# Kernel optimization log

Hardware: AMD Instinct MI355X
Metric: run time of the kernel (lower is better)

The kernel has to match this reference:

```python
import jax, jax.numpy as jnp
import numpy as np
import math

D_MODEL = 1024
N_HEADS = 16
HEAD_DIM = D_MODEL // N_HEADS
SEQ_LEN = 8192
INCLUDE_LOCAL = 2


def get_dilated_positions(seq_len, include_local=2):
    # Faithful numpy port of the torch pattern generator (runs once at setup).
    max_attend = include_local + int(math.ceil(math.log2(seq_len + 1)))
    positions = np.zeros((seq_len, max_attend), dtype=np.int64)
    mask = np.zeros((seq_len, max_attend), dtype=bool)
    for i in range(seq_len):
        ap = [i]
        for j in range(1, include_local + 1):
            if i - j >= 0:
                ap.append(i - j)
        k = 2
        while i - 2 ** k >= 0:
            ap.append(i - 2 ** k)
            k += 1
        positions[i, :len(ap)] = ap
        mask[i, :len(ap)] = True
    return positions, mask


def setup_inputs() -> dict:
    key = jax.random.key(0)
    kx, kq, kk, kv, ko = jax.random.split(key, 5)
    x = jax.random.normal(kx, (1, SEQ_LEN, D_MODEL), dtype=jnp.float32)
    # nn.Linear(bias=False) weights, torch layout [out_features, in_features]
    s = 0.02
    q_w = jax.random.normal(kq, (D_MODEL, D_MODEL), dtype=jnp.float32) * s
    k_w = jax.random.normal(kk, (D_MODEL, D_MODEL), dtype=jnp.float32) * s
    v_w = jax.random.normal(kv, (D_MODEL, D_MODEL), dtype=jnp.float32) * s
    o_w = jax.random.normal(ko, (D_MODEL, D_MODEL), dtype=jnp.float32) * s
    pos_np, mask_np = get_dilated_positions(SEQ_LEN, INCLUDE_LOCAL)
    return {
        "x": x,
        "q_w": q_w, "k_w": k_w, "v_w": v_w, "o_w": o_w,
        "positions": jnp.asarray(pos_np),   # (S, A) int64 indices
        "attend_mask": jnp.asarray(mask_np) # (S, A) bool
    }


def reference(x, q_w, k_w, v_w, o_w, positions, attend_mask):
    B, S, _ = x.shape
    H, Dh = N_HEADS, HEAD_DIM
    scale = Dh ** -0.5

    q = (x @ q_w.T).reshape(B, S, H, Dh).transpose(0, 2, 1, 3)  # (B,H,S,Dh)
    k = (x @ k_w.T).reshape(B, S, H, Dh).transpose(0, 2, 1, 3)
    v = (x @ v_w.T).reshape(B, S, H, Dh).transpose(0, 2, 1, 3)

    # Gather K/V at the dilated positions: (B,H,S,A,Dh)
    k_sparse = k[:, :, positions, :]
    v_sparse = v[:, :, positions, :]

    scores = jnp.einsum('bhsd,bhsad->bhsa', q, k_sparse) * scale
    scores = jnp.where(attend_mask[None, None, :, :], scores, -jnp.inf)
    attn = jax.nn.softmax(scores, axis=-1)  # dropout p in eval / 0.0 -> identity

    out = jnp.einsum('bhsa,bhsad->bhsd', attn, v_sparse)
    out = out.transpose(0, 2, 1, 3).reshape(B, S, D_MODEL)
    return out @ o_w.T
```

## Files before the change

### kernel.cpp

```cpp
#include <hip/hip_runtime.h>
#include <hip/hip_bf16.h>

typedef __bf16 bf16_t;
typedef __bf16 bf16x4 __attribute__((ext_vector_type(4)));
typedef __bf16 bf16x8 __attribute__((ext_vector_type(8)));
typedef float floatx4 __attribute__((ext_vector_type(4)));

#define SEQ    8192
#define DM     1024
#define NHEADS 16
#define HDIM   64

__device__ __forceinline__ void async_ld16(bf16_t* lds, const bf16_t* g) {
  __builtin_amdgcn_global_load_lds(
      (__attribute__((address_space(1))) void*)g,
      (__attribute__((address_space(3))) void*)lds, 16, 0, 0);
}

__global__ __launch_bounds__(256)
void cvt_all(const float* __restrict__ x,  const float* __restrict__ qw,
             const float* __restrict__ kw, const float* __restrict__ vw,
             const float* __restrict__ ow,
             bf16_t* __restrict__ Xb,  bf16_t* __restrict__ QWb,
             bf16_t* __restrict__ KWb, bf16_t* __restrict__ VWb,
             bf16_t* __restrict__ OWb) {
  const int b = blockIdx.x;
  const float* in; bf16_t* out; int g;
  if (b < 8192) { in = x; out = Xb; g = b; }
  else {
    const int w  = (b - 8192) >> 10;
    const int wb = (b - 8192) & 1023;
    switch (w) {
      case 0:  in = qw; out = QWb; break;
      case 1:  in = kw; out = KWb; break;
      case 2:  in = vw; out = VWb; break;
      default: in = ow; out = OWb; break;
    }
    g = wb;
  }
  const int idx = (g * 256 + threadIdx.x) * 4;
  float4 v = *(const float4*)(in + idx);
  bf16x4 o = { (bf16_t)v.x, (bf16_t)v.y, (bf16_t)v.z, (bf16_t)v.w };
  *(bf16x4*)(out + idx) = o;
}


__global__ __launch_bounds__(256)
void gemm_qkv(const bf16_t* __restrict__ A,
              const bf16_t* __restrict__ Bq, const bf16_t* __restrict__ Bk,
              const bf16_t* __restrict__ Bv,
              bf16_t* __restrict__ Cq, bf16_t* __restrict__ Ck, bf16_t* __restrict__ Cv)
{
  const bf16_t* B = (blockIdx.z == 0) ? Bq : (blockIdx.z == 1) ? Bk : Bv;
  bf16_t*       C = (blockIdx.z == 0) ? Cq : (blockIdx.z == 1) ? Ck : Cv;
  constexpr int Kdim = DM;
  __shared__ __attribute__((aligned(16))) bf16_t sA[128 * 32];
  __shared__ __attribute__((aligned(16))) bf16_t sB[128 * 32];

  const int tid  = threadIdx.x;
  const int wave = tid >> 6;
  const int lane = tid & 63;
  const int quad = lane >> 4;
  const int r16  = lane & 15;
  const int wr   = (wave >> 1) * 64;
  const int wc   = (wave & 1) * 64;

  const int gc = (lane & 3) ^ ((lane >> 3) & 3);
  const size_t arow0 = (size_t)blockIdx.x * 128 + wave * 32 + (lane >> 2);
  const size_t brow0 = (size_t)blockIdx.y * 128 + wave * 32 + (lane >> 2);
  const bf16_t* Ag = A + arow0 * Kdim + gc * 8;
  const bf16_t* Bg = B + brow0 * Kdim + gc * 8;
  bf16_t* sAw = sA + wave * 32 * 32;
  bf16_t* sBw = sB + wave * 32 * 32;

  const int slotA = ((quad ^ ((r16 >> 1) & 3)) * 8);

  floatx4 acc[4][4];
  #pragma unroll
  for (int i = 0; i < 4; ++i)
    #pragma unroll
    for (int j = 0; j < 4; ++j)
      acc[i][j] = (floatx4)(0.0f);

  for (int ko = 0; ko < Kdim; ko += 32) {
    async_ld16(sAw,           Ag + ko);
    async_ld16(sAw + 16 * 32, Ag + 16 * Kdim + ko);
    async_ld16(sBw,           Bg + ko);
    async_ld16(sBw + 16 * 32, Bg + 16 * Kdim + ko);
    __syncthreads();

    bf16x8 af[4], bfr[4];
    #pragma unroll
    for (int mi = 0; mi < 4; ++mi)
      af[mi] = *(const bf16x8*)&sA[(wr + mi * 16 + r16) * 32 + slotA];
    #pragma unroll
    for (int ni = 0; ni < 4; ++ni)
      bfr[ni] = *(const bf16x8*)&sB[(wc + ni * 16 + r16) * 32 + slotA];

    #pragma unroll
    for (int mi = 0; mi < 4; ++mi)
      #pragma unroll
      for (int ni = 0; ni < 4; ++ni)
        acc[mi][ni] = __builtin_amdgcn_mfma_f32_16x16x32_bf16(af[mi], bfr[ni], acc[mi][ni], 0, 0, 0);

    __syncthreads();
  }

  const float scl = (blockIdx.z == 0) ? 0.125f : 1.0f;
  const int crow0 = blockIdx.x * 128 + wr + quad * 4;
  const int ccol0 = blockIdx.y * 128 + wc + r16;
  #pragma unroll
  for (int mi = 0; mi < 4; ++mi)
    #pragma unroll
    for (int ni = 0; ni < 4; ++ni)
      #pragma unroll
      for (int r = 0; r < 4; ++r)
        C[(size_t)(crow0 + mi * 16 + r) * DM + (ccol0 + ni * 16)] = (bf16_t)(acc[mi][ni][r] * scl);
}

__global__ __launch_bounds__(256)
void gemm_out(const bf16_t* __restrict__ A, const bf16_t* __restrict__ B,
              float* __restrict__ C)
{
  constexpr int Kdim = DM;
  __shared__ __attribute__((aligned(16))) bf16_t sA[128 * 32];
  __shared__ __attribute__((aligned(16))) bf16_t sB[64 * 32];

  const int tid  = threadIdx.x;
  const int wave = tid >> 6;
  const int lane = tid & 63;
  const int quad = lane >> 4;
  const int r16  = lane & 15;
  const int wr   = (wave >> 1) * 64;
  const int wc   = (wave & 1) * 32;

  const int gc = (lane & 3) ^ ((lane >> 3) & 3);
  const size_t arow = (size_t)blockIdx.x * 128 + wave * 32 + (lane >> 2);
  const size_t brow = (size_t)blockIdx.y * 64 + wave * 16 + (lane >> 2);
  const bf16_t* Ag = A + arow * Kdim + gc * 8;
  const bf16_t* Bg = B + brow * Kdim + gc * 8;
  bf16_t* sAw = sA + wave * 32 * 32;
  bf16_t* sBw = sB + wave * 16 * 32;

  const int slotA = ((quad ^ ((r16 >> 1) & 3)) * 8);

  floatx4 acc[4][2];
  #pragma unroll
  for (int i = 0; i < 4; ++i)
    #pragma unroll
    for (int j = 0; j < 2; ++j)
      acc[i][j] = (floatx4)(0.0f);

  for (int ko = 0; ko < Kdim; ko += 32) {
    async_ld16(sAw,           Ag + ko);
    async_ld16(sAw + 16 * 32, Ag + 16 * Kdim + ko);
    async_ld16(sBw,           Bg + ko);
    __syncthreads();

    bf16x8 af[4], bfr[2];
    #pragma unroll
    for (int mi = 0; mi < 4; ++mi)
      af[mi] = *(const bf16x8*)&sA[(wr + mi * 16 + r16) * 32 + slotA];
    #pragma unroll
    for (int ni = 0; ni < 2; ++ni)
      bfr[ni] = *(const bf16x8*)&sB[(wc + ni * 16 + r16) * 32 + slotA];

    #pragma unroll
    for (int mi = 0; mi < 4; ++mi)
      #pragma unroll
      for (int ni = 0; ni < 2; ++ni)
        acc[mi][ni] = __builtin_amdgcn_mfma_f32_16x16x32_bf16(af[mi], bfr[ni], acc[mi][ni], 0, 0, 0);

    __syncthreads();
  }

  const int crow0 = blockIdx.x * 128 + wr + quad * 4;
  const int ccol0 = blockIdx.y * 64 + wc + r16;
  #pragma unroll
  for (int mi = 0; mi < 4; ++mi)
    #pragma unroll
    for (int ni = 0; ni < 2; ++ni)
      #pragma unroll
      for (int r = 0; r < 4; ++r)
        C[(size_t)(crow0 + mi * 16 + r) * DM + (ccol0 + ni * 16)] = acc[mi][ni][r];
}

__global__ __launch_bounds__(256)
void dilated_attn(const bf16_t* __restrict__ Q, const bf16_t* __restrict__ K,
                  const bf16_t* __restrict__ V, bf16_t* O)
{
  const int lane = threadIdx.x & 63;
  const int qb   = (blockIdx.x & 7) * 256 + (blockIdx.x >> 3);
  const int i    = qb * 4 + (threadIdx.x >> 6);
  const size_t base = (size_t)i * DM + lane * 16;

  bf16x8 q0 = *(const bf16x8*)(Q + base);
  bf16x8 q1 = *(const bf16x8*)(Q + base + 8);
  float qf[16];
  #pragma unroll
  for (int j = 0; j < 8; ++j) { qf[j] = (float)q0[j]; qf[j + 8] = (float)q1[j]; }

  float m = -INFINITY, l = 0.0f;
  float acc[16];
  #pragma unroll
  for (int j = 0; j < 16; ++j) acc[j] = 0.0f;

  int off = 1;
  bf16x8 k0 = *(const bf16x8*)(K + base), k1 = *(const bf16x8*)(K + base + 8);
  bf16x8 v0 = *(const bf16x8*)(V + base), v1 = *(const bf16x8*)(V + base + 8);

  while (true) {
    const int pn = i - off;
    const bool more = (pn >= 0);
    bf16x8 nk0, nk1, nv0, nv1;
    if (more) {
      size_t nb = (size_t)pn * DM + lane * 16;
      nk0 = *(const bf16x8*)(K + nb); nk1 = *(const bf16x8*)(K + nb + 8);
      nv0 = *(const bf16x8*)(V + nb); nv1 = *(const bf16x8*)(V + nb + 8);
    }

    float sc = 0.0f;
    #pragma unroll
    for (int j = 0; j < 8; ++j) sc += qf[j] * (float)k0[j] + qf[j + 8] * (float)k1[j];
    sc += __shfl_xor(sc, 1, 64);
    sc += __shfl_xor(sc, 2, 64);

    float mn = fmaxf(m, sc);
    float co = __expf(m - mn);
    float w  = __expf(sc - mn);
    l = l * co + w;
    m = mn;
    #pragma unroll
    for (int j = 0; j < 8; ++j) {
      acc[j]     = acc[j]     * co + w * (float)v0[j];
      acc[j + 8] = acc[j + 8] * co + w * (float)v1[j];
    }

    if (!more) break;
    k0 = nk0; k1 = nk1; v0 = nv0; v1 = nv1;
    off <<= 1;
  }

  const float inv = 1.0f / l;
  bf16x8 o0, o1;
  #pragma unroll
  for (int j = 0; j < 8; ++j) { o0[j] = (bf16_t)(acc[j] * inv); o1[j] = (bf16_t)(acc[j + 8] * inv); }
  *(bf16x8*)(O + base)     = o0;
  *(bf16x8*)(O + base + 8) = o1;
}

extern "C" void kernel_launch(void* const* d_in, const int* in_sizes, int n_in,
                              void* d_out, int out_size, void* d_ws, size_t ws_size,
                              hipStream_t stream) {
  (void)in_sizes; (void)n_in; (void)out_size; (void)ws_size;
  const float* x  = (const float*)d_in[0];
  const float* qw = (const float*)d_in[1];
  const float* kw = (const float*)d_in[2];
  const float* vw = (const float*)d_in[3];
  const float* ow = (const float*)d_in[4];
  float* out = (float*)d_out;

  bf16_t* Xb  = (bf16_t*)d_ws;
  bf16_t* Qb  = Xb  + (size_t)SEQ * DM;
  bf16_t* Kb  = Qb  + (size_t)SEQ * DM;
  bf16_t* Vb  = Kb  + (size_t)SEQ * DM;
  bf16_t* QWb = Vb  + (size_t)SEQ * DM;
  bf16_t* KWb = QWb + (size_t)DM * DM;
  bf16_t* VWb = KWb + (size_t)DM * DM;
  bf16_t* OWb = VWb + (size_t)DM * DM;
  bf16_t* AO  = Qb;

  cvt_all<<<dim3(8192 + 4096), dim3(256), 0, stream>>>(x, qw, kw, vw, ow,
                                                       Xb, QWb, KWb, VWb, OWb);

  dim3 block(256);
  gemm_qkv<<<dim3(SEQ / 128, DM / 128, 3), block, 0, stream>>>(Xb, QWb, KWb, VWb, Qb, Kb, Vb);
  dilated_attn<<<dim3(SEQ / 4), block, 0, stream>>>(Qb, Kb, Vb, AO);
  gemm_out<<<dim3(SEQ / 128, DM / 64), block, 0, stream>>>(AO, OWb, out);
}
```

Before: 224.3 us.

## Widen output GEMM tile to 128x128 and double-buffer dilated attention K/V loads

The output projection GEMM now uses 128x128 block tiles instead of 128x64, so each wave computes a 64x64 sub-tile with a 4x4 grid of MFMA accumulators. This halves the number of blocks and gives more reuse of the loaded A rows. The dilated attention loop now computes the position count up front from the leading-zero count and keeps two K/V register buffers, prefetching two positions ahead to hide gather latency. The cost is higher register pressure in both kernels and fewer blocks for the GEMM to spread across CUs.

```diff
diff --git a/kernel.cpp b/kernel.cpp
--- a/kernel.cpp
+++ b/kernel.cpp
@@ -124,7 +124,7 @@
 {
   constexpr int Kdim = DM;
   __shared__ __attribute__((aligned(16))) bf16_t sA[128 * 32];
-  __shared__ __attribute__((aligned(16))) bf16_t sB[64 * 32];
+  __shared__ __attribute__((aligned(16))) bf16_t sB[128 * 32];
 
   const int tid  = threadIdx.x;
   const int wave = tid >> 6;
@@ -132,54 +132,55 @@
   const int quad = lane >> 4;
   const int r16  = lane & 15;
   const int wr   = (wave >> 1) * 64;
-  const int wc   = (wave & 1) * 32;
+  const int wc   = (wave & 1) * 64;
 
   const int gc = (lane & 3) ^ ((lane >> 3) & 3);
-  const size_t arow = (size_t)blockIdx.x * 128 + wave * 32 + (lane >> 2);
-  const size_t brow = (size_t)blockIdx.y * 64 + wave * 16 + (lane >> 2);
-  const bf16_t* Ag = A + arow * Kdim + gc * 8;
-  const bf16_t* Bg = B + brow * Kdim + gc * 8;
+  const size_t arow0 = (size_t)blockIdx.x * 128 + wave * 32 + (lane >> 2);
+  const size_t brow0 = (size_t)blockIdx.y * 128 + wave * 32 + (lane >> 2);
+  const bf16_t* Ag = A + arow0 * Kdim + gc * 8;
+  const bf16_t* Bg = B + brow0 * Kdim + gc * 8;
   bf16_t* sAw = sA + wave * 32 * 32;
-  bf16_t* sBw = sB + wave * 16 * 32;
+  bf16_t* sBw = sB + wave * 32 * 32;
 
   const int slotA = ((quad ^ ((r16 >> 1) & 3)) * 8);
 
-  floatx4 acc[4][2];
+  floatx4 acc[4][4];
   #pragma unroll
   for (int i = 0; i < 4; ++i)
     #pragma unroll
-    for (int j = 0; j < 2; ++j)
+    for (int j = 0; j < 4; ++j)
       acc[i][j] = (floatx4)(0.0f);
 
   for (int ko = 0; ko < Kdim; ko += 32) {
     async_ld16(sAw,           Ag + ko);
     async_ld16(sAw + 16 * 32, Ag + 16 * Kdim + ko);
     async_ld16(sBw,           Bg + ko);
+    async_ld16(sBw + 16 * 32, Bg + 16 * Kdim + ko);
     __syncthreads();
 
-    bf16x8 af[4], bfr[2];
+    bf16x8 af[4], bfr[4];
     #pragma unroll
     for (int mi = 0; mi < 4; ++mi)
       af[mi] = *(const bf16x8*)&sA[(wr + mi * 16 + r16) * 32 + slotA];
     #pragma unroll
-    for (int ni = 0; ni < 2; ++ni)
+    for (int ni = 0; ni < 4; ++ni)
       bfr[ni] = *(const bf16x8*)&sB[(wc + ni * 16 + r16) * 32 + slotA];
 
     #pragma unroll
     for (int mi = 0; mi < 4; ++mi)
       #pragma unroll
-      for (int ni = 0; ni < 2; ++ni)
+      for (int ni = 0; ni < 4; ++ni)
         acc[mi][ni] = __builtin_amdgcn_mfma_f32_16x16x32_bf16(af[mi], bfr[ni], acc[mi][ni], 0, 0, 0);
 
     __syncthreads();
   }
 
   const int crow0 = blockIdx.x * 128 + wr + quad * 4;
-  const int ccol0 = blockIdx.y * 64 + wc + r16;
+  const int ccol0 = blockIdx.y * 128 + wc + r16;
   #pragma unroll
   for (int mi = 0; mi < 4; ++mi)
     #pragma unroll
-    for (int ni = 0; ni < 2; ++ni)
+    for (int ni = 0; ni < 4; ++ni)
       #pragma unroll
       for (int r = 0; r < 4; ++r)
         C[(size_t)(crow0 + mi * 16 + r) * DM + (ccol0 + ni * 16)] = acc[mi][ni][r];
@@ -200,46 +201,67 @@
   #pragma unroll
   for (int j = 0; j < 8; ++j) { qf[j] = (float)q0[j]; qf[j + 8] = (float)q1[j]; }
 
+  const int npos = (i == 0) ? 1 : (33 - __builtin_clz((unsigned)i));
+  auto pos_addr = [&](int t) -> size_t {
+    const int off = (t == 0) ? 0 : (1 << (t - 1));
+    return (size_t)(i - off) * DM + lane * 16;
+  };
+
   float m = -INFINITY, l = 0.0f;
   float acc[16];
   #pragma unroll
   for (int j = 0; j < 16; ++j) acc[j] = 0.0f;
 
-  int off = 1;
-  bf16x8 k0 = *(const bf16x8*)(K + base), k1 = *(const bf16x8*)(K + base + 8);
-  bf16x8 v0 = *(const bf16x8*)(V + base), v1 = *(const bf16x8*)(V + base + 8);
-
+  bf16x8 ka0, ka1, va0, va1, kb0 = {}, kb1 = {}, vb0 = {}, vb1 = {};
+  {
+    ka0 = *(const bf16x8*)(K + base); ka1 = *(const bf16x8*)(K + base + 8);
+    va0 = *(const bf16x8*)(V + base); va1 = *(const bf16x8*)(V + base + 8);
+  }
+  if (npos > 1) {
+    const size_t a = pos_addr(1);
+    kb0 = *(const bf16x8*)(K + a); kb1 = *(const bf16x8*)(K + a + 8);
+    vb0 = *(const bf16x8*)(V + a); vb1 = *(const bf16x8*)(V + a + 8);
+  }
+
+#define ATTN_STEP(K0, K1, V0, V1)                                              \
+  {                                                                            \
+    float sc = 0.0f;                                                           \
+    _Pragma("unroll")                                                          \
+    for (int j = 0; j < 8; ++j)                                                \
+      sc += qf[j] * (float)K0[j] + qf[j + 8] * (float)K1[j];                   \
+    sc += __shfl_xor(sc, 1, 64);                                               \
+    sc += __shfl_xor(sc, 2, 64);                                               \
+    float mn = fmaxf(m, sc);                                                   \
+    float co = __expf(m - mn);                                                 \
+    float w  = __expf(sc - mn);                                                \
+    l = l * co + w;                                                            \
+    m = mn;                                                                    \
+    _Pragma("unroll")                                                          \
+    for (int j = 0; j < 8; ++j) {                                              \
+      acc[j]     = acc[j]     * co + w * (float)V0[j];                         \
+      acc[j + 8] = acc[j + 8] * co + w * (float)V1[j];                         \
+    }                                                                          \
+  }
+
+  int t = 0;
   while (true) {
-    const int pn = i - off;
-    const bool more = (pn >= 0);
-    bf16x8 nk0, nk1, nv0, nv1;
-    if (more) {
-      size_t nb = (size_t)pn * DM + lane * 16;
-      nk0 = *(const bf16x8*)(K + nb); nk1 = *(const bf16x8*)(K + nb + 8);
-      nv0 = *(const bf16x8*)(V + nb); nv1 = *(const bf16x8*)(V + nb + 8);
+    ATTN_STEP(ka0, ka1, va0, va1);
+    if (t + 2 < npos) {
+      const size_t a = pos_addr(t + 2);
+      ka0 = *(const bf16x8*)(K + a); ka1 = *(const bf16x8*)(K + a + 8);
+      va0 = *(const bf16x8*)(V + a); va1 = *(const bf16x8*)(V + a + 8);
     }
-
-    float sc = 0.0f;
-    #pragma unroll
-    for (int j = 0; j < 8; ++j) sc += qf[j] * (float)k0[j] + qf[j + 8] * (float)k1[j];
-    sc += __shfl_xor(sc, 1, 64);
-    sc += __shfl_xor(sc, 2, 64);
-
-    float mn = fmaxf(m, sc);
-    float co = __expf(m - mn);
-    float w  = __expf(sc - mn);
-    l = l * co + w;
-    m = mn;
-    #pragma unroll
-    for (int j = 0; j < 8; ++j) {
-      acc[j]     = acc[j]     * co + w * (float)v0[j];
-      acc[j + 8] = acc[j + 8] * co + w * (float)v1[j];
+    if (++t >= npos) break;
+
+    ATTN_STEP(kb0, kb1, vb0, vb1);
+    if (t + 2 < npos) {
+      const size_t a = pos_addr(t + 2);
+      kb0 = *(const bf16x8*)(K + a); kb1 = *(const bf16x8*)(K + a + 8);
+      vb0 = *(const bf16x8*)(V + a); vb1 = *(const bf16x8*)(V + a + 8);
     }
-
-    if (!more) break;
-    k0 = nk0; k1 = nk1; v0 = nv0; v1 = nv1;
-    off <<= 1;
-  }
+    if (++t >= npos) break;
+  }
+#undef ATTN_STEP
 
   const float inv = 1.0f / l;
   bf16x8 o0, o1;
@@ -276,5 +298,5 @@
   dim3 block(256);
   gemm_qkv<<<dim3(SEQ / 128, DM / 128, 3), block, 0, stream>>>(Xb, QWb, KWb, VWb, Qb, Kb, Vb);
   dilated_attn<<<dim3(SEQ / 4), block, 0, stream>>>(Qb, Kb, Vb, AO);
-  gemm_out<<<dim3(SEQ / 128, DM / 64), block, 0, stream>>>(AO, OWb, out);
-}
+  gemm_out<<<dim3(SEQ / 128, DM / 128), block, 0, stream>>>(AO, OWb, out);
+}
```

After: 221.9 us. No clear change (-1.0%).

## Split dilated attention positions across two waves and enlarge output GEMM tile

Applied to the files above, without the earlier changes.

Each query's dilated key/value positions are split between two waves, each keeping its own running softmax state. The two partial states are merged through shared memory with a block barrier. This halves the serial dependent-load chain per wave and doubles the number of waves. Separately, the output projection GEMM tile grows from 128x64 to 128x128 for more operand reuse per block, at the cost of more accumulator registers and half as many blocks.

```diff
diff --git a/kernel.cpp b/kernel.cpp
--- a/kernel.cpp
+++ b/kernel.cpp
@@ -124,7 +124,7 @@
 {
   constexpr int Kdim = DM;
   __shared__ __attribute__((aligned(16))) bf16_t sA[128 * 32];
-  __shared__ __attribute__((aligned(16))) bf16_t sB[64 * 32];
+  __shared__ __attribute__((aligned(16))) bf16_t sB[128 * 32];
 
   const int tid  = threadIdx.x;
   const int wave = tid >> 6;
@@ -132,54 +132,55 @@
   const int quad = lane >> 4;
   const int r16  = lane & 15;
   const int wr   = (wave >> 1) * 64;
-  const int wc   = (wave & 1) * 32;
+  const int wc   = (wave & 1) * 64;
 
   const int gc = (lane & 3) ^ ((lane >> 3) & 3);
-  const size_t arow = (size_t)blockIdx.x * 128 + wave * 32 + (lane >> 2);
-  const size_t brow = (size_t)blockIdx.y * 64 + wave * 16 + (lane >> 2);
-  const bf16_t* Ag = A + arow * Kdim + gc * 8;
-  const bf16_t* Bg = B + brow * Kdim + gc * 8;
+  const size_t arow0 = (size_t)blockIdx.x * 128 + wave * 32 + (lane >> 2);
+  const size_t brow0 = (size_t)blockIdx.y * 128 + wave * 32 + (lane >> 2);
+  const bf16_t* Ag = A + arow0 * Kdim + gc * 8;
+  const bf16_t* Bg = B + brow0 * Kdim + gc * 8;
   bf16_t* sAw = sA + wave * 32 * 32;
-  bf16_t* sBw = sB + wave * 16 * 32;
+  bf16_t* sBw = sB + wave * 32 * 32;
 
   const int slotA = ((quad ^ ((r16 >> 1) & 3)) * 8);
 
-  floatx4 acc[4][2];
+  floatx4 acc[4][4];
   #pragma unroll
   for (int i = 0; i < 4; ++i)
     #pragma unroll
-    for (int j = 0; j < 2; ++j)
+    for (int j = 0; j < 4; ++j)
       acc[i][j] = (floatx4)(0.0f);
 
   for (int ko = 0; ko < Kdim; ko += 32) {
     async_ld16(sAw,           Ag + ko);
     async_ld16(sAw + 16 * 32, Ag + 16 * Kdim + ko);
     async_ld16(sBw,           Bg + ko);
+    async_ld16(sBw + 16 * 32, Bg + 16 * Kdim + ko);
     __syncthreads();
 
-    bf16x8 af[4], bfr[2];
+    bf16x8 af[4], bfr[4];
     #pragma unroll
     for (int mi = 0; mi < 4; ++mi)
       af[mi] = *(const bf16x8*)&sA[(wr + mi * 16 + r16) * 32 + slotA];
     #pragma unroll
-    for (int ni = 0; ni < 2; ++ni)
+    for (int ni = 0; ni < 4; ++ni)
       bfr[ni] = *(const bf16x8*)&sB[(wc + ni * 16 + r16) * 32 + slotA];
 
     #pragma unroll
     for (int mi = 0; mi < 4; ++mi)
       #pragma unroll
-      for (int ni = 0; ni < 2; ++ni)
+      for (int ni = 0; ni < 4; ++ni)
         acc[mi][ni] = __builtin_amdgcn_mfma_f32_16x16x32_bf16(af[mi], bfr[ni], acc[mi][ni], 0, 0, 0);
 
     __syncthreads();
   }
 
   const int crow0 = blockIdx.x * 128 + wr + quad * 4;
-  const int ccol0 = blockIdx.y * 64 + wc + r16;
+  const int ccol0 = blockIdx.y * 128 + wc + r16;
   #pragma unroll
   for (int mi = 0; mi < 4; ++mi)
     #pragma unroll
-    for (int ni = 0; ni < 2; ++ni)
+    for (int ni = 0; ni < 4; ++ni)
       #pragma unroll
       for (int r = 0; r < 4; ++r)
         C[(size_t)(crow0 + mi * 16 + r) * DM + (ccol0 + ni * 16)] = acc[mi][ni][r];
@@ -189,9 +190,16 @@
 void dilated_attn(const bf16_t* __restrict__ Q, const bf16_t* __restrict__ K,
                   const bf16_t* __restrict__ V, bf16_t* O)
 {
+  __shared__ float sM[2][64];
+  __shared__ float sL[2][64];
+  __shared__ float sAcc[2][64][17];
+
   const int lane = threadIdx.x & 63;
-  const int qb   = (blockIdx.x & 7) * 256 + (blockIdx.x >> 3);
-  const int i    = qb * 4 + (threadIdx.x >> 6);
+  const int wv   = threadIdx.x >> 6;
+  const int ql   = wv >> 1;
+  const int sub  = wv & 1;
+  const int qb   = (blockIdx.x & 7) * 512 + (blockIdx.x >> 3);
+  const int i    = qb * 2 + ql;
   const size_t base = (size_t)i * DM + lane * 16;
 
   bf16x8 q0 = *(const bf16x8*)(Q + base);
@@ -200,53 +208,77 @@
   #pragma unroll
   for (int j = 0; j < 8; ++j) { qf[j] = (float)q0[j]; qf[j + 8] = (float)q1[j]; }
 
+  const int npos = (i == 0) ? 1 : (33 - __builtin_clz((unsigned)i));
+  auto pos_addr = [&](int t) -> size_t {
+    const int off = (t == 0) ? 0 : (1 << (t - 1));
+    return (size_t)(i - off) * DM + lane * 16;
+  };
+
   float m = -INFINITY, l = 0.0f;
   float acc[16];
   #pragma unroll
   for (int j = 0; j < 16; ++j) acc[j] = 0.0f;
 
-  int off = 1;
-  bf16x8 k0 = *(const bf16x8*)(K + base), k1 = *(const bf16x8*)(K + base + 8);
-  bf16x8 v0 = *(const bf16x8*)(V + base), v1 = *(const bf16x8*)(V + base + 8);
-
-  while (true) {
-    const int pn = i - off;
-    const bool more = (pn >= 0);
-    bf16x8 nk0, nk1, nv0, nv1;
-    if (more) {
-      size_t nb = (size_t)pn * DM + lane * 16;
-      nk0 = *(const bf16x8*)(K + nb); nk1 = *(const bf16x8*)(K + nb + 8);
-      nv0 = *(const bf16x8*)(V + nb); nv1 = *(const bf16x8*)(V + nb + 8);
+  int t = sub;
+  if (t < npos) {
+    size_t a = pos_addr(t);
+    bf16x8 k0 = *(const bf16x8*)(K + a), k1 = *(const bf16x8*)(K + a + 8);
+    bf16x8 v0 = *(const bf16x8*)(V + a), v1 = *(const bf16x8*)(V + a + 8);
+    while (true) {
+      const int tn = t + 2;
+      const bool more = (tn < npos);
+      bf16x8 nk0, nk1, nv0, nv1;
+      if (more) {
+        const size_t na = pos_addr(tn);
+        nk0 = *(const bf16x8*)(K + na); nk1 = *(const bf16x8*)(K + na + 8);
+        nv0 = *(const bf16x8*)(V + na); nv1 = *(const bf16x8*)(V + na + 8);
+      }
+
+      float sc = 0.0f;
+      #pragma unroll
+      for (int j = 0; j < 8; ++j) sc += qf[j] * (float)k0[j] + qf[j + 8] * (float)k1[j];
+      sc += __shfl_xor(sc, 1, 64);
+      sc += __shfl_xor(sc, 2, 64);
+
+      float mn = fmaxf(m, sc);
+      float co = __expf(m - mn);
+      float w  = __expf(sc - mn);
+      l = l * co + w;
+      m = mn;
+      #pragma unroll
+      for (int j = 0; j < 8; ++j) {
+        acc[j]     = acc[j]     * co + w * (float)v0[j];
+        acc[j + 8] = acc[j + 8] * co + w * (float)v1[j];
+      }
+
+      if (!more) break;
+      k0 = nk0; k1 = nk1; v0 = nv0; v1 = nv1;
+      t = tn;
     }
-
-    float sc = 0.0f;
-    #pragma unroll
-    for (int j = 0; j < 8; ++j) sc += qf[j] * (float)k0[j] + qf[j + 8] * (float)k1[j];
-    sc += __shfl_xor(sc, 1, 64);
-    sc += __shfl_xor(sc, 2, 64);
-
-    float mn = fmaxf(m, sc);
-    float co = __expf(m - mn);
-    float w  = __expf(sc - mn);
-    l = l * co + w;
-    m = mn;
+  }
+
+  if (sub == 1) {
+    sM[ql][lane] = m;
+    sL[ql][lane] = l;
+    #pragma unroll
+    for (int j = 0; j < 16; ++j) sAcc[ql][lane][j] = acc[j];
+  }
+  __syncthreads();
+  if (sub == 0) {
+    const float mb = sM[ql][lane], lb = sL[ql][lane];
+    const float mt = fmaxf(m, mb);
+    const float ca = __expf(m - mt);
+    const float cb = __expf(mb - mt);
+    const float inv = 1.0f / (l * ca + lb * cb);
+    bf16x8 o0, o1;
     #pragma unroll
     for (int j = 0; j < 8; ++j) {
-      acc[j]     = acc[j]     * co + w * (float)v0[j];
-      acc[j + 8] = acc[j + 8] * co + w * (float)v1[j];
+      o0[j] = (bf16_t)((acc[j]     * ca + sAcc[ql][lane][j]     * cb) * inv);
+      o1[j] = (bf16_t)((acc[j + 8] * ca + sAcc[ql][lane][j + 8] * cb) * inv);
     }
-
-    if (!more) break;
-    k0 = nk0; k1 = nk1; v0 = nv0; v1 = nv1;
-    off <<= 1;
-  }
-
-  const float inv = 1.0f / l;
-  bf16x8 o0, o1;
-  #pragma unroll
-  for (int j = 0; j < 8; ++j) { o0[j] = (bf16_t)(acc[j] * inv); o1[j] = (bf16_t)(acc[j + 8] * inv); }
-  *(bf16x8*)(O + base)     = o0;
-  *(bf16x8*)(O + base + 8) = o1;
+    *(bf16x8*)(O + base)     = o0;
+    *(bf16x8*)(O + base + 8) = o1;
+  }
 }
 
 extern "C" void kernel_launch(void* const* d_in, const int* in_sizes, int n_in,
@@ -275,6 +307,6 @@
 
   dim3 block(256);
   gemm_qkv<<<dim3(SEQ / 128, DM / 128, 3), block, 0, stream>>>(Xb, QWb, KWb, VWb, Qb, Kb, Vb);
-  dilated_attn<<<dim3(SEQ / 4), block, 0, stream>>>(Qb, Kb, Vb, AO);
-  gemm_out<<<dim3(SEQ / 128, DM / 64), block, 0, stream>>>(AO, OWb, out);
-}
+  dilated_attn<<<dim3(SEQ / 2), block, 0, stream>>>(Qb, Kb, Vb, AO);
+  gemm_out<<<dim3(SEQ / 128, DM / 128), block, 0, stream>>>(AO, OWb, out);
+}
```

New measurement: 220.8 us. No clear change (-1.5%).
